# Kernel tuning notes

Hardware: AMD Instinct MI355X
Metric: run time of the kernel (lower is better)

Reference implementation:

```python
import jax, jax.numpy as jnp
import numpy as np

NROW = 200000
R = 32
B = 131072
NDIM = 3
STEP = 0.01  # stepsize from optimize() default step=lambda x: 0.01


def setup_inputs() -> dict:
    key = jax.random.key(0)
    ks = jax.random.split(key, 12)
    inp = {}
    for d in range(NDIM):
        # positive entries (like torch.rand) keep phi > 0
        inp[f"U{d}"] = jax.random.uniform(ks[d], (NROW, R), dtype=jnp.float32, minval=0.05, maxval=1.0)
        inp[f"S{d}"] = jax.random.uniform(ks[3 + d], (NROW, R), dtype=jnp.float32)
        inp[f"T{d}"] = jax.random.uniform(ks[6 + d], (NROW, R), dtype=jnp.float32)
    inp["L"] = jax.random.uniform(ks[9], (R,), dtype=jnp.float32, minval=0.1, maxval=1.0)
    inp["batch_vals"] = jax.random.randint(ks[10], (B,), 0, 2).astype(jnp.float32)  # binary data
    inp["batch_entries"] = jax.random.randint(ks[11], (B, NDIM), 0, NROW)
    return inp


def _em_update(U, S, T, L, batch_vals, batch_entries):
    # U, S, T: (ndim, nrow, R); batch_entries: (B, ndim); batch_vals: (B,)
    idx = batch_entries.T  # (ndim, B)
    g = jax.vmap(lambda u, i: u[i])(U, idx)  # gathered rows: (ndim, B, R)
    # c_vectors[dim] = L * prod of OTHER dims' gathered vectors
    prod_others = jnp.stack([g[1] * g[2], g[0] * g[2], g[0] * g[1]])  # (ndim, B, R)
    c = L * prod_others  # (ndim, B, R)
    p = g[0] * g[1] * g[2]  # (B, R) full elementwise product
    phi = jnp.sum(L * p, axis=-1)  # (B,)
    # d_vectors[dim, b, r] = phi[b] - L[r] * p[b, r]  (same for every dim)
    d_vec = (phi[:, None] - L * p)[None]  # (1, B, R)
    # expectation step (binary): E[wi] = 0.5/phi * tanh(phi/2)
    wi = 0.5 / phi * jnp.tanh(phi / 2.0)  # (B,)
    ki = batch_vals - 0.5  # (B,)
    wi_b = wi[None, :, None]
    s_upd = c * c * wi_b  # (ndim, B, R)
    t_upd = (ki[None, :, None] - d_vec * wi_b) * c  # (ndim, B, R)
    seg = lambda dat, i: jax.ops.segment_sum(dat, i, num_segments=NROW)
    s_acc = jax.vmap(seg)(s_upd, idx)  # (ndim, NROW, R)
    t_acc = jax.vmap(seg)(t_upd, idx)
    cnt = jax.vmap(seg)(jnp.ones(idx.shape, jnp.float32), idx)  # (ndim, NROW)
    touched = (cnt > 0)[..., None]
    # EMA write-back only to rows that appeared in the batch
    S_new = jnp.where(touched, (1.0 - STEP) * S + STEP * s_acc, S)
    T_new = jnp.where(touched, (1.0 - STEP) * T + STEP * t_acc, T)
    return jnp.stack([S_new, T_new])  # (2, ndim, NROW, R)


def reference(U0, U1, U2, S0, S1, S2, T0, T1, T2, L, batch_vals, batch_entries):
    U = jnp.stack([U0, U1, U2])
    S = jnp.stack([S0, S1, S2])
    T = jnp.stack([T0, T1, T2])
    return _em_update(U, S, T, L, batch_vals, batch_entries)
```

## Files before the change

### kernel.cpp

```cpp
#include <hip/hip_runtime.h>

#define NROW 200000
#define RDIM 32
#define BATCH 131072
#define STEP 0.01f
#define CAPB 4
#define ROWS3 (3 * NROW)


__device__ __forceinline__ unsigned f2bf(float x) {
    unsigned u = __float_as_uint(x);
    return (u + 0x8000u) >> 16;
}
__device__ __forceinline__ float bf2f(unsigned h) {
    return __uint_as_float(h << 16);
}

__global__ __launch_bounds__(256) void em_pre_v11(
    const float* __restrict__ U0, const float* __restrict__ U1,
    const float* __restrict__ U2, const float* __restrict__ L,
    const float* __restrict__ bv, const int* __restrict__ be,
    int* __restrict__ cnt, int* __restrict__ head, int* __restrict__ nxt,
    int* __restrict__ bucket2, float2* __restrict__ scal, float* __restrict__ LpBuf)
{
    int tid = blockIdx.x * blockDim.x + threadIdx.x;
    int i   = tid >> 3;
    int sub = tid & 7;
    if (i >= BATCH) return;

    int e0 = be[i * 3 + 0];
    int e1 = be[i * 3 + 1];
    int e2 = be[i * 3 + 2];

    float4 g0 = *(const float4*)(U0 + (size_t)e0 * RDIM + sub * 4);
    float4 g1 = *(const float4*)(U1 + (size_t)e1 * RDIM + sub * 4);
    float4 g2 = *(const float4*)(U2 + (size_t)e2 * RDIM + sub * 4);
    float4 Lv = *(const float4*)(L + sub * 4);

    float4 Lp;
    Lp.x = Lv.x * g0.x * g1.x * g2.x;
    Lp.y = Lv.y * g0.y * g1.y * g2.y;
    Lp.z = Lv.z * g0.z * g1.z * g2.z;
    Lp.w = Lv.w * g0.w * g1.w * g2.w;

    float phi = (Lp.x + Lp.y) + (Lp.z + Lp.w);
    phi += __shfl_xor(phi, 1);
    phi += __shfl_xor(phi, 2);
    phi += __shfl_xor(phi, 4);

    float wi = 0.5f / phi * tanhf(0.5f * phi);
    float A  = (bv[i] - 0.5f) - phi * wi;

    *(float4*)(LpBuf + (size_t)i * RDIM + sub * 4) = Lp;

    if (sub == 0) scal[i] = make_float2(A, wi);

    if (sub < 3) {
        int row  = (sub == 0) ? e0 : (sub == 1) ? e1 : e2;
        int rid  = sub * NROW + row;
        int slot = atomicAdd(&cnt[rid], 1);
        if (slot < CAPB) {
            int packed = (int)((f2bf(A) << 16) | f2bf(wi));
            *(int2*)(bucket2 + (size_t)rid * 8 + slot * 2) = make_int2(i, packed);
        } else {
            int idx = i * 3 + sub;
            nxt[idx] = atomicExch(&head[rid], idx + 1);
        }
    }
}

#define ACCS(SA, TA, RG, Aj, Wj, P)                                     \
{                                                                       \
    float cx = (P).x * (RG).x, cy = (P).y * (RG).y,                     \
          cz = (P).z * (RG).z, cw = (P).w * (RG).w;                     \
    (SA).x += (Wj) * cx * cx;  (SA).y += (Wj) * cy * cy;                \
    (SA).z += (Wj) * cz * cz;  (SA).w += (Wj) * cw * cw;                \
    (TA).x += ((Aj) + (Wj) * (P).x) * cx;                               \
    (TA).y += ((Aj) + (Wj) * (P).y) * cy;                               \
    (TA).z += ((Aj) + (Wj) * (P).z) * cz;                               \
    (TA).w += ((Aj) + (Wj) * (P).w) * cw;                               \
}

__global__ __launch_bounds__(256) void em_apply_v11(
    const float* __restrict__ U0, const float* __restrict__ U1,
    const float* __restrict__ U2,
    const float* __restrict__ S0, const float* __restrict__ S1,
    const float* __restrict__ S2,
    const float* __restrict__ T0, const float* __restrict__ T1,
    const float* __restrict__ T2,
    const int* __restrict__ cnt, const int* __restrict__ head,
    const int* __restrict__ nxt, const int* __restrict__ bucket2,
    const float2* __restrict__ scal, const float* __restrict__ LpBuf,
    float* __restrict__ out)
{
    int tid = blockIdx.x * blockDim.x + threadIdx.x;
    int rid = tid >> 3;
    int sub = tid & 7;
    if (rid >= ROWS3) return;

    int d   = rid / NROW;
    int row = rid - d * NROW;

    const float* Ud   = (d == 0) ? U0 : (d == 1) ? U1 : U2;
    const float* Ssrc = (d == 0) ? S0 : (d == 1) ? S1 : S2;
    const float* Tsrc = (d == 0) ? T0 : (d == 1) ? T1 : T2;

    size_t roff = (size_t)row * RDIM + sub * 4;

    int    n    = cnt[rid];
    const int* brow = bucket2 + (size_t)rid * 8;
    int4   b01  = *(const int4*)(brow);
    int4   b23  = *(const int4*)(brow + 4);
    float4 s_in = *(const float4*)(Ssrc + roff);
    float4 t_in = *(const float4*)(Tsrc + roff);

    int i0 = (n > 0) ? b01.x : 0;
    int i1 = (n > 1) ? b01.z : 0;
    int i2 = (n > 2) ? b23.x : 0;
    int i3 = (n > 3) ? b23.z : 0;

    float4 p0 = *(const float4*)(LpBuf + (size_t)i0 * RDIM + sub * 4);
    float4 p1 = *(const float4*)(LpBuf + (size_t)i1 * RDIM + sub * 4);
    float4 p2 = *(const float4*)(LpBuf + (size_t)i2 * RDIM + sub * 4);
    float4 p3 = *(const float4*)(LpBuf + (size_t)i3 * RDIM + sub * 4);

    float A0 = bf2f(((unsigned)b01.y) >> 16), W0 = bf2f(((unsigned)b01.y) & 0xffffu);
    float A1 = bf2f(((unsigned)b01.w) >> 16), W1 = bf2f(((unsigned)b01.w) & 0xffffu);
    float A2 = bf2f(((unsigned)b23.y) >> 16), W2 = bf2f(((unsigned)b23.y) & 0xffffu);
    float A3 = bf2f(((unsigned)b23.w) >> 16), W3 = bf2f(((unsigned)b23.w) & 0xffffu);
    if (n <= 1) { A1 = 0.f; W1 = 0.f; }
    if (n <= 2) { A2 = 0.f; W2 = 0.f; }
    if (n <= 3) { A3 = 0.f; W3 = 0.f; }

    float4 rg = make_float4(0.f, 0.f, 0.f, 0.f);
    if (n > 0) {
        float4 gd = *(const float4*)(Ud + roff);
        rg.x = __builtin_amdgcn_rcpf(gd.x);
        rg.y = __builtin_amdgcn_rcpf(gd.y);
        rg.z = __builtin_amdgcn_rcpf(gd.z);
        rg.w = __builtin_amdgcn_rcpf(gd.w);
    }

    float4 sa = make_float4(0.f, 0.f, 0.f, 0.f);
    float4 ta = make_float4(0.f, 0.f, 0.f, 0.f);

    ACCS(sa, ta, rg, A0, W0, p0)
    ACCS(sa, ta, rg, A1, W1, p1)
    ACCS(sa, ta, rg, A2, W2, p2)
    ACCS(sa, ta, rg, A3, W3, p3)

    if (n > CAPB) {
        int t = head[rid];
        while (t != 0) {
            int idx = t - 1;
            int e   = idx / 3;
            float2 aw = scal[e];
            float4 P  = *(const float4*)(LpBuf + (size_t)e * RDIM + sub * 4);
            ACCS(sa, ta, rg, aw.x, aw.y, P)
            t = nxt[idx];
        }
    }

    bool touched = (n > 0);
    float4 oS, oT;
    oS.x = touched ? (1.0f - STEP) * s_in.x + STEP * sa.x : s_in.x;
    oS.y = touched ? (1.0f - STEP) * s_in.y + STEP * sa.y : s_in.y;
    oS.z = touched ? (1.0f - STEP) * s_in.z + STEP * sa.z : s_in.z;
    oS.w = touched ? (1.0f - STEP) * s_in.w + STEP * sa.w : s_in.w;
    oT.x = touched ? (1.0f - STEP) * t_in.x + STEP * ta.x : t_in.x;
    oT.y = touched ? (1.0f - STEP) * t_in.y + STEP * ta.y : t_in.y;
    oT.z = touched ? (1.0f - STEP) * t_in.z + STEP * ta.z : t_in.z;
    oT.w = touched ? (1.0f - STEP) * t_in.w + STEP * ta.w : t_in.w;

    size_t off = (size_t)rid * RDIM + sub * 4;
    *(float4*)(out + off) = oS;
    *(float4*)(out + (size_t)ROWS3 * RDIM + off) = oT;
}

__global__ __launch_bounds__(256) void em_pre(
    const float* __restrict__ U0, const float* __restrict__ U1,
    const float* __restrict__ U2, const float* __restrict__ L,
    const float* __restrict__ bv, const int* __restrict__ be,
    int* __restrict__ head, int* __restrict__ nxt,
    float2* __restrict__ scal, float* __restrict__ LpBuf)
{
    int tid = blockIdx.x * blockDim.x + threadIdx.x;
    int i   = tid >> 3;
    int sub = tid & 7;
    if (i >= BATCH) return;

    int e0 = be[i * 3 + 0];
    int e1 = be[i * 3 + 1];
    int e2 = be[i * 3 + 2];

    float4 g0 = *(const float4*)(U0 + (size_t)e0 * RDIM + sub * 4);
    float4 g1 = *(const float4*)(U1 + (size_t)e1 * RDIM + sub * 4);
    float4 g2 = *(const float4*)(U2 + (size_t)e2 * RDIM + sub * 4);
    float4 Lv = *(const float4*)(L + sub * 4);

    float4 Lp;
    Lp.x = Lv.x * g0.x * g1.x * g2.x;
    Lp.y = Lv.y * g0.y * g1.y * g2.y;
    Lp.z = Lv.z * g0.z * g1.z * g2.z;
    Lp.w = Lv.w * g0.w * g1.w * g2.w;

    float phi = (Lp.x + Lp.y) + (Lp.z + Lp.w);
    phi += __shfl_xor(phi, 1);
    phi += __shfl_xor(phi, 2);
    phi += __shfl_xor(phi, 4);

    float wi = 0.5f / phi * tanhf(0.5f * phi);

    *(float4*)(LpBuf + (size_t)i * RDIM + sub * 4) = Lp;

    if (sub == 0) {
        float A = (bv[i] - 0.5f) - phi * wi;
        scal[i] = make_float2(A, wi);
    }
    if (sub < 3) {
        int row = (sub == 0) ? e0 : (sub == 1) ? e1 : e2;
        int idx = i * 3 + sub;
        nxt[idx] = atomicExch(&head[sub * NROW + row], idx + 1);
    }
}

__global__ __launch_bounds__(256) void em_apply_vec(
    const float* __restrict__ U0, const float* __restrict__ U1,
    const float* __restrict__ U2,
    const float* __restrict__ S0, const float* __restrict__ S1,
    const float* __restrict__ S2,
    const float* __restrict__ T0, const float* __restrict__ T1,
    const float* __restrict__ T2,
    const int* __restrict__ head, const int* __restrict__ nxt,
    const float2* __restrict__ scal, const float* __restrict__ LpBuf,
    float* __restrict__ out)
{
    int tid = blockIdx.x * blockDim.x + threadIdx.x;
    int rid = tid >> 3;
    int sub = tid & 7;
    if (rid >= ROWS3) return;

    int d   = rid / NROW;
    int row = rid - d * NROW;

    const float* Ud   = (d == 0) ? U0 : (d == 1) ? U1 : U2;
    const float* Ssrc = (d == 0) ? S0 : (d == 1) ? S1 : S2;
    const float* Tsrc = (d == 0) ? T0 : (d == 1) ? T1 : T2;

    size_t roff = (size_t)row * RDIM + sub * 4;
    float4 s_in = *(const float4*)(Ssrc + roff);
    float4 t_in = *(const float4*)(Tsrc + roff);

    int    t  = head[rid];
    float4 oS = s_in;
    float4 oT = t_in;

    if (t != 0) {
        float4 gd = *(const float4*)(Ud + roff);
        float4 rg;
        rg.x = __builtin_amdgcn_rcpf(gd.x);
        rg.y = __builtin_amdgcn_rcpf(gd.y);
        rg.z = __builtin_amdgcn_rcpf(gd.z);
        rg.w = __builtin_amdgcn_rcpf(gd.w);

        float4 sa = make_float4(0.f, 0.f, 0.f, 0.f);
        float4 ta = make_float4(0.f, 0.f, 0.f, 0.f);
        while (t != 0) {
            int idx = t - 1;
            int e = idx / 3;
            float2 aw = scal[e];
            float4 Lp = *(const float4*)(LpBuf + (size_t)e * RDIM + sub * 4);
            ACCS(sa, ta, rg, aw.x, aw.y, Lp)
            t = nxt[idx];
        }
        oS.x = (1.0f - STEP) * s_in.x + STEP * sa.x;
        oS.y = (1.0f - STEP) * s_in.y + STEP * sa.y;
        oS.z = (1.0f - STEP) * s_in.z + STEP * sa.z;
        oS.w = (1.0f - STEP) * s_in.w + STEP * sa.w;
        oT.x = (1.0f - STEP) * t_in.x + STEP * ta.x;
        oT.y = (1.0f - STEP) * t_in.y + STEP * ta.y;
        oT.z = (1.0f - STEP) * t_in.z + STEP * ta.z;
        oT.w = (1.0f - STEP) * t_in.w + STEP * ta.w;
    }

    size_t offS = (size_t)rid * RDIM + sub * 4;
    *(float4*)(out + offS) = oS;
    *(float4*)(out + (size_t)ROWS3 * RDIM + offS) = oT;
}

extern "C" void kernel_launch(void* const* d_in, const int* in_sizes, int n_in,
                              void* d_out, int out_size, void* d_ws, size_t ws_size,
                              hipStream_t stream)
{
    const float* U0 = (const float*)d_in[0];
    const float* S0 = (const float*)d_in[1];
    const float* T0 = (const float*)d_in[2];
    const float* U1 = (const float*)d_in[3];
    const float* S1 = (const float*)d_in[4];
    const float* T1 = (const float*)d_in[5];
    const float* U2 = (const float*)d_in[6];
    const float* S2 = (const float*)d_in[7];
    const float* T2 = (const float*)d_in[8];
    const float* L  = (const float*)d_in[9];
    const float* bv = (const float*)d_in[10];
    const int*   be = (const int*)d_in[11];

    float* out = (float*)d_out;

    const size_t rows3 = (size_t)ROWS3;
    const size_t nxt_n = (size_t)3 * BATCH;
    const size_t bk2_n = rows3 * 8;

    const size_t ws_fast = (2 * rows3 + nxt_n + bk2_n) * sizeof(int)
                         + (size_t)BATCH * sizeof(float2)
                         + (size_t)BATCH * RDIM * sizeof(float);
    const size_t ws_mid  = (rows3 + nxt_n) * sizeof(int)
                         + (size_t)BATCH * sizeof(float2)
                         + (size_t)BATCH * RDIM * sizeof(float);

    if (ws_size >= ws_fast) {
        int*    cnt     = (int*)d_ws;
        int*    head_   = cnt + rows3;
        int*    nxt     = head_ + rows3;
        int*    bucket2 = nxt + nxt_n;
        float2* scal    = (float2*)(bucket2 + bk2_n);
        float*  LpBuf   = (float*)(scal + BATCH);

        hipMemsetAsync(cnt, 0, 2 * rows3 * sizeof(int), stream);

        int pblocks = (BATCH * 8 + 255) / 256;
        em_pre_v11<<<pblocks, 256, 0, stream>>>(U0, U1, U2, L, bv, be,
                                                cnt, head_, nxt, bucket2,
                                                scal, LpBuf);

        long athreads = (long)ROWS3 * 8;
        int  ablocks  = (int)((athreads + 255) / 256);
        em_apply_v11<<<ablocks, 256, 0, stream>>>(U0, U1, U2, S0, S1, S2,
                                                  T0, T1, T2, cnt, head_, nxt,
                                                  bucket2, scal, LpBuf, out);
    } else if (ws_size >= ws_mid) {
        int*    head_ = (int*)d_ws;
        int*    nxt   = head_ + rows3;
        float2* scal  = (float2*)(nxt + nxt_n);
        float*  LpBuf = (float*)(scal + BATCH);

        hipMemsetAsync(head_, 0, rows3 * sizeof(int), stream);

        int pblocks = (BATCH * 8 + 255) / 256;
        em_pre<<<pblocks, 256, 0, stream>>>(U0, U1, U2, L, bv, be,
                                            head_, nxt, scal, LpBuf);

        long athreads = (long)ROWS3 * 8;
        int  ablocks  = (int)((athreads + 255) / 256);
        em_apply_vec<<<ablocks, 256, 0, stream>>>(U0, U1, U2, S0, S1, S2,
                                                  T0, T1, T2, head_, nxt,
                                                  scal, LpBuf, out);
    }
}
```

Baseline: 107.0 us.

## Precompute per-entry bf16 S/T contributions into fat buckets in pre kernel

The pre kernel now computes the full per-entry S and T contributions (wi*c^2 and (A+wi*Lp)*c) for the first CAPB occurrences of each row. It stores them packed as bf16 pairs in a fat per-row bucket array. The apply kernel then just sums up to four uint4 loads per lane and skips the U reload and reciprocal unless a row overflows into the linked list. This trades a much larger workspace (rows3*CAPB*128 bytes) and extra bf16 rounding of the contributions for less gather-dependent work in the apply pass. It only takes effect if the provided workspace is large enough.

```diff
diff --git a/kernel.cpp b/kernel.cpp
--- a/kernel.cpp
+++ b/kernel.cpp
@@ -12,8 +12,184 @@
     unsigned u = __float_as_uint(x);
     return (u + 0x8000u) >> 16;
 }
-__device__ __forceinline__ float bf2f(unsigned h) {
-    return __uint_as_float(h << 16);
+__device__ __forceinline__ float bf2f(unsigned h) { return __uint_as_float(h << 16); }
+__device__ __forceinline__ float bfhi(unsigned u) { return __uint_as_float(u & 0xffff0000u); }
+__device__ __forceinline__ float bflo(unsigned u) { return __uint_as_float(u << 16); }
+__device__ __forceinline__ unsigned pk2(float hi, float lo) {
+    return (f2bf(hi) << 16) | f2bf(lo);
+}
+
+#define ACCS(SA, TA, RG, Aj, Wj, P)                                     \
+{                                                                       \
+    float cx = (P).x * (RG).x, cy = (P).y * (RG).y,                     \
+          cz = (P).z * (RG).z, cw = (P).w * (RG).w;                     \
+    (SA).x += (Wj) * cx * cx;  (SA).y += (Wj) * cy * cy;                \
+    (SA).z += (Wj) * cz * cz;  (SA).w += (Wj) * cw * cw;                \
+    (TA).x += ((Aj) + (Wj) * (P).x) * cx;                               \
+    (TA).y += ((Aj) + (Wj) * (P).y) * cy;                               \
+    (TA).z += ((Aj) + (Wj) * (P).z) * cz;                               \
+    (TA).w += ((Aj) + (Wj) * (P).w) * cw;                               \
+}
+
+__global__ __launch_bounds__(256) void em_pre_v12(
+    const float* __restrict__ U0, const float* __restrict__ U1,
+    const float* __restrict__ U2, const float* __restrict__ L,
+    const float* __restrict__ bv, const int* __restrict__ be,
+    int* __restrict__ cnt, int* __restrict__ head, int* __restrict__ nxt,
+    float2* __restrict__ scal, float* __restrict__ LpBuf,
+    unsigned* __restrict__ fat)
+{
+    int tid = blockIdx.x * blockDim.x + threadIdx.x;
+    int i   = tid >> 3;
+    int sub = tid & 7;
+    if (i >= BATCH) return;
+
+    int e0 = be[i * 3 + 0];
+    int e1 = be[i * 3 + 1];
+    int e2 = be[i * 3 + 2];
+
+    float4 g0 = *(const float4*)(U0 + (size_t)e0 * RDIM + sub * 4);
+    float4 g1 = *(const float4*)(U1 + (size_t)e1 * RDIM + sub * 4);
+    float4 g2 = *(const float4*)(U2 + (size_t)e2 * RDIM + sub * 4);
+    float4 Lv = *(const float4*)(L + sub * 4);
+
+    float4 Lp;
+    Lp.x = Lv.x * g0.x * g1.x * g2.x;
+    Lp.y = Lv.y * g0.y * g1.y * g2.y;
+    Lp.z = Lv.z * g0.z * g1.z * g2.z;
+    Lp.w = Lv.w * g0.w * g1.w * g2.w;
+
+    float phi = (Lp.x + Lp.y) + (Lp.z + Lp.w);
+    phi += __shfl_xor(phi, 1);
+    phi += __shfl_xor(phi, 2);
+    phi += __shfl_xor(phi, 4);
+
+    float wi = 0.5f / phi * tanhf(0.5f * phi);
+    float A  = (bv[i] - 0.5f) - phi * wi;
+
+    *(float4*)(LpBuf + (size_t)i * RDIM + sub * 4) = Lp;
+    if (sub == 0) scal[i] = make_float2(A, wi);
+
+    int slotv = 0;
+    if (sub < 3) {
+        int row = (sub == 0) ? e0 : (sub == 1) ? e1 : e2;
+        int rid = sub * NROW + row;
+        slotv = atomicAdd(&cnt[rid], 1);
+        if (slotv >= CAPB) {
+            int idx = i * 3 + sub;
+            nxt[idx] = atomicExch(&head[rid], idx + 1);
+        }
+    }
+    int s0 = __shfl(slotv, 0, 8);
+    int s1 = __shfl(slotv, 1, 8);
+    int s2 = __shfl(slotv, 2, 8);
+
+    float4 tc;
+    tc.x = A + wi * Lp.x;  tc.y = A + wi * Lp.y;
+    tc.z = A + wi * Lp.z;  tc.w = A + wi * Lp.w;
+
+    #define EMIT(SLOT, RID, CA, CB)                                         \
+    if ((SLOT) < CAPB) {                                                    \
+        float4 c;                                                           \
+        c.x = Lv.x * (CA).x * (CB).x;  c.y = Lv.y * (CA).y * (CB).y;        \
+        c.z = Lv.z * (CA).z * (CB).z;  c.w = Lv.w * (CA).w * (CB).w;        \
+        uint4 q;                                                            \
+        q.x = pk2(wi * c.x * c.x, wi * c.y * c.y);                          \
+        q.y = pk2(wi * c.z * c.z, wi * c.w * c.w);                          \
+        q.z = pk2(tc.x * c.x, tc.y * c.y);                                  \
+        q.w = pk2(tc.z * c.z, tc.w * c.w);                                  \
+        *(uint4*)(fat + ((size_t)(RID) * CAPB + (SLOT)) * 32 + sub * 4) = q;\
+    }
+
+    EMIT(s0, 0 * NROW + e0, g1, g2)
+    EMIT(s1, 1 * NROW + e1, g0, g2)
+    EMIT(s2, 2 * NROW + e2, g0, g1)
+    #undef EMIT
+}
+
+__global__ __launch_bounds__(256) void em_apply_v12(
+    const float* __restrict__ U0, const float* __restrict__ U1,
+    const float* __restrict__ U2,
+    const float* __restrict__ S0, const float* __restrict__ S1,
+    const float* __restrict__ S2,
+    const float* __restrict__ T0, const float* __restrict__ T1,
+    const float* __restrict__ T2,
+    const int* __restrict__ cnt, const int* __restrict__ head,
+    const int* __restrict__ nxt, const unsigned* __restrict__ fat,
+    const float2* __restrict__ scal, const float* __restrict__ LpBuf,
+    float* __restrict__ out)
+{
+    int tid = blockIdx.x * blockDim.x + threadIdx.x;
+    int rid = tid >> 3;
+    int sub = tid & 7;
+    if (rid >= ROWS3) return;
+
+    int d   = rid / NROW;
+    int row = rid - d * NROW;
+
+    const float* Ssrc = (d == 0) ? S0 : (d == 1) ? S1 : S2;
+    const float* Tsrc = (d == 0) ? T0 : (d == 1) ? T1 : T2;
+
+    size_t roff = (size_t)row * RDIM + sub * 4;
+
+    int    n    = cnt[rid];
+    float4 s_in = *(const float4*)(Ssrc + roff);
+    float4 t_in = *(const float4*)(Tsrc + roff);
+
+    const unsigned* fb = fat + (size_t)rid * CAPB * 32 + sub * 4;
+    uint4 q0 = make_uint4(0, 0, 0, 0);
+    uint4 q1 = q0, q2 = q0, q3 = q0;
+    if (n > 0) q0 = *(const uint4*)(fb);
+    if (n > 1) q1 = *(const uint4*)(fb + 32);
+    if (n > 2) q2 = *(const uint4*)(fb + 64);
+    if (n > 3) q3 = *(const uint4*)(fb + 96);
+
+    float4 sa = make_float4(0.f, 0.f, 0.f, 0.f);
+    float4 ta = make_float4(0.f, 0.f, 0.f, 0.f);
+
+    #define UACC(Q)                                         \
+    {                                                       \
+        sa.x += bfhi((Q).x);  sa.y += bflo((Q).x);          \
+        sa.z += bfhi((Q).y);  sa.w += bflo((Q).y);          \
+        ta.x += bfhi((Q).z);  ta.y += bflo((Q).z);          \
+        ta.z += bfhi((Q).w);  ta.w += bflo((Q).w);          \
+    }
+    UACC(q0) UACC(q1) UACC(q2) UACC(q3)
+    #undef UACC
+
+    if (n > CAPB) {
+        const float* Ud = (d == 0) ? U0 : (d == 1) ? U1 : U2;
+        float4 gd = *(const float4*)(Ud + roff);
+        float4 rg;
+        rg.x = __builtin_amdgcn_rcpf(gd.x);
+        rg.y = __builtin_amdgcn_rcpf(gd.y);
+        rg.z = __builtin_amdgcn_rcpf(gd.z);
+        rg.w = __builtin_amdgcn_rcpf(gd.w);
+        int t = head[rid];
+        while (t != 0) {
+            int idx = t - 1;
+            int e   = idx / 3;
+            float2 aw = scal[e];
+            float4 P  = *(const float4*)(LpBuf + (size_t)e * RDIM + sub * 4);
+            ACCS(sa, ta, rg, aw.x, aw.y, P)
+            t = nxt[idx];
+        }
+    }
+
+    bool touched = (n > 0);
+    float4 oS, oT;
+    oS.x = touched ? (1.0f - STEP) * s_in.x + STEP * sa.x : s_in.x;
+    oS.y = touched ? (1.0f - STEP) * s_in.y + STEP * sa.y : s_in.y;
+    oS.z = touched ? (1.0f - STEP) * s_in.z + STEP * sa.z : s_in.z;
+    oS.w = touched ? (1.0f - STEP) * s_in.w + STEP * sa.w : s_in.w;
+    oT.x = touched ? (1.0f - STEP) * t_in.x + STEP * ta.x : t_in.x;
+    oT.y = touched ? (1.0f - STEP) * t_in.y + STEP * ta.y : t_in.y;
+    oT.z = touched ? (1.0f - STEP) * t_in.z + STEP * ta.z : t_in.z;
+    oT.w = touched ? (1.0f - STEP) * t_in.w + STEP * ta.w : t_in.w;
+
+    size_t off = (size_t)rid * RDIM + sub * 4;
+    *(float4*)(out + off) = oS;
+    *(float4*)(out + (size_t)ROWS3 * RDIM + off) = oT;
 }
 
 __global__ __launch_bounds__(256) void em_pre_v11(
@@ -67,18 +243,6 @@
             nxt[idx] = atomicExch(&head[rid], idx + 1);
         }
     }
-}
-
-#define ACCS(SA, TA, RG, Aj, Wj, P)                                     \
-{                                                                       \
-    float cx = (P).x * (RG).x, cy = (P).y * (RG).y,                     \
-          cz = (P).z * (RG).z, cw = (P).w * (RG).w;                     \
-    (SA).x += (Wj) * cx * cx;  (SA).y += (Wj) * cy * cy;                \
-    (SA).z += (Wj) * cz * cz;  (SA).w += (Wj) * cw * cw;                \
-    (TA).x += ((Aj) + (Wj) * (P).x) * cx;                               \
-    (TA).y += ((Aj) + (Wj) * (P).y) * cy;                               \
-    (TA).z += ((Aj) + (Wj) * (P).z) * cz;                               \
-    (TA).w += ((Aj) + (Wj) * (P).w) * cw;                               \
 }
 
 __global__ __launch_bounds__(256) void em_apply_v11(
@@ -177,117 +341,6 @@
     *(float4*)(out + (size_t)ROWS3 * RDIM + off) = oT;
 }
 
-__global__ __launch_bounds__(256) void em_pre(
-    const float* __restrict__ U0, const float* __restrict__ U1,
-    const float* __restrict__ U2, const float* __restrict__ L,
-    const float* __restrict__ bv, const int* __restrict__ be,
-    int* __restrict__ head, int* __restrict__ nxt,
-    float2* __restrict__ scal, float* __restrict__ LpBuf)
-{
-    int tid = blockIdx.x * blockDim.x + threadIdx.x;
-    int i   = tid >> 3;
-    int sub = tid & 7;
-    if (i >= BATCH) return;
-
-    int e0 = be[i * 3 + 0];
-    int e1 = be[i * 3 + 1];
-    int e2 = be[i * 3 + 2];
-
-    float4 g0 = *(const float4*)(U0 + (size_t)e0 * RDIM + sub * 4);
-    float4 g1 = *(const float4*)(U1 + (size_t)e1 * RDIM + sub * 4);
-    float4 g2 = *(const float4*)(U2 + (size_t)e2 * RDIM + sub * 4);
-    float4 Lv = *(const float4*)(L + sub * 4);
-
-    float4 Lp;
-    Lp.x = Lv.x * g0.x * g1.x * g2.x;
-    Lp.y = Lv.y * g0.y * g1.y * g2.y;
-    Lp.z = Lv.z * g0.z * g1.z * g2.z;
-    Lp.w = Lv.w * g0.w * g1.w * g2.w;
-
-    float phi = (Lp.x + Lp.y) + (Lp.z + Lp.w);
-    phi += __shfl_xor(phi, 1);
-    phi += __shfl_xor(phi, 2);
-    phi += __shfl_xor(phi, 4);
-
-    float wi = 0.5f / phi * tanhf(0.5f * phi);
-
-    *(float4*)(LpBuf + (size_t)i * RDIM + sub * 4) = Lp;
-
-    if (sub == 0) {
-        float A = (bv[i] - 0.5f) - phi * wi;
-        scal[i] = make_float2(A, wi);
-    }
-    if (sub < 3) {
-        int row = (sub == 0) ? e0 : (sub == 1) ? e1 : e2;
-        int idx = i * 3 + sub;
-        nxt[idx] = atomicExch(&head[sub * NROW + row], idx + 1);
-    }
-}
-
-__global__ __launch_bounds__(256) void em_apply_vec(
-    const float* __restrict__ U0, const float* __restrict__ U1,
-    const float* __restrict__ U2,
-    const float* __restrict__ S0, const float* __restrict__ S1,
-    const float* __restrict__ S2,
-    const float* __restrict__ T0, const float* __restrict__ T1,
-    const float* __restrict__ T2,
-    const int* __restrict__ head, const int* __restrict__ nxt,
-    const float2* __restrict__ scal, const float* __restrict__ LpBuf,
-    float* __restrict__ out)
-{
-    int tid = blockIdx.x * blockDim.x + threadIdx.x;
-    int rid = tid >> 3;
-    int sub = tid & 7;
-    if (rid >= ROWS3) return;
-
-    int d   = rid / NROW;
-    int row = rid - d * NROW;
-
-    const float* Ud   = (d == 0) ? U0 : (d == 1) ? U1 : U2;
-    const float* Ssrc = (d == 0) ? S0 : (d == 1) ? S1 : S2;
-    const float* Tsrc = (d == 0) ? T0 : (d == 1) ? T1 : T2;
-
-    size_t roff = (size_t)row * RDIM + sub * 4;
-    float4 s_in = *(const float4*)(Ssrc + roff);
-    float4 t_in = *(const float4*)(Tsrc + roff);
-
-    int    t  = head[rid];
-    float4 oS = s_in;
-    float4 oT = t_in;
-
-    if (t != 0) {
-        float4 gd = *(const float4*)(Ud + roff);
-        float4 rg;
-        rg.x = __builtin_amdgcn_rcpf(gd.x);
-        rg.y = __builtin_amdgcn_rcpf(gd.y);
-        rg.z = __builtin_amdgcn_rcpf(gd.z);
-        rg.w = __builtin_amdgcn_rcpf(gd.w);
-
-        float4 sa = make_float4(0.f, 0.f, 0.f, 0.f);
-        float4 ta = make_float4(0.f, 0.f, 0.f, 0.f);
-        while (t != 0) {
-            int idx = t - 1;
-            int e = idx / 3;
-            float2 aw = scal[e];
-            float4 Lp = *(const float4*)(LpBuf + (size_t)e * RDIM + sub * 4);
-            ACCS(sa, ta, rg, aw.x, aw.y, Lp)
-            t = nxt[idx];
-        }
-        oS.x = (1.0f - STEP) * s_in.x + STEP * sa.x;
-        oS.y = (1.0f - STEP) * s_in.y + STEP * sa.y;
-        oS.z = (1.0f - STEP) * s_in.z + STEP * sa.z;
-        oS.w = (1.0f - STEP) * s_in.w + STEP * sa.w;
-        oT.x = (1.0f - STEP) * t_in.x + STEP * ta.x;
-        oT.y = (1.0f - STEP) * t_in.y + STEP * ta.y;
-        oT.z = (1.0f - STEP) * t_in.z + STEP * ta.z;
-        oT.w = (1.0f - STEP) * t_in.w + STEP * ta.w;
-    }
-
-    size_t offS = (size_t)rid * RDIM + sub * 4;
-    *(float4*)(out + offS) = oS;
-    *(float4*)(out + (size_t)ROWS3 * RDIM + offS) = oT;
-}
-
 extern "C" void kernel_launch(void* const* d_in, const int* in_sizes, int n_in,
                               void* d_out, int out_size, void* d_ws, size_t ws_size,
                               hipStream_t stream)
@@ -309,16 +362,36 @@
 
     const size_t rows3 = (size_t)ROWS3;
     const size_t nxt_n = (size_t)3 * BATCH;
-    const size_t bk2_n = rows3 * 8;
-
-    const size_t ws_fast = (2 * rows3 + nxt_n + bk2_n) * sizeof(int)
-                         + (size_t)BATCH * sizeof(float2)
-                         + (size_t)BATCH * RDIM * sizeof(float);
-    const size_t ws_mid  = (rows3 + nxt_n) * sizeof(int)
-                         + (size_t)BATCH * sizeof(float2)
-                         + (size_t)BATCH * RDIM * sizeof(float);
-
-    if (ws_size >= ws_fast) {
+
+    const size_t ws_v12 = (2 * rows3 + nxt_n) * sizeof(int)
+                        + (size_t)BATCH * sizeof(float2)
+                        + (size_t)BATCH * RDIM * sizeof(float)
+                        + rows3 * CAPB * 32 * sizeof(unsigned);
+    const size_t bk2_n  = rows3 * 8;
+    const size_t ws_v11 = (2 * rows3 + nxt_n + bk2_n) * sizeof(int)
+                        + (size_t)BATCH * sizeof(float2)
+                        + (size_t)BATCH * RDIM * sizeof(float);
+
+    int pblocks = (BATCH * 8 + 255) / 256;
+    long athreads = (long)ROWS3 * 8;
+    int  ablocks  = (int)((athreads + 255) / 256);
+
+    if (ws_size >= ws_v12) {
+        int*      cnt   = (int*)d_ws;
+        int*      head_ = cnt + rows3;
+        int*      nxt   = head_ + rows3;
+        float2*   scal  = (float2*)(nxt + nxt_n);
+        float*    LpBuf = (float*)(scal + BATCH);
+        unsigned* fat   = (unsigned*)(LpBuf + (size_t)BATCH * RDIM);
+
+        hipMemsetAsync(cnt, 0, 2 * rows3 * sizeof(int), stream);
+
+        em_pre_v12<<<pblocks, 256, 0, stream>>>(U0, U1, U2, L, bv, be,
+                                                cnt, head_, nxt, scal, LpBuf, fat);
+        em_apply_v12<<<ablocks, 256, 0, stream>>>(U0, U1, U2, S0, S1, S2,
+                                                  T0, T1, T2, cnt, head_, nxt,
+                                                  fat, scal, LpBuf, out);
+    } else if (ws_size >= ws_v11) {
         int*    cnt     = (int*)d_ws;
         int*    head_   = cnt + rows3;
         int*    nxt     = head_ + rows3;
@@ -328,32 +401,11 @@
 
         hipMemsetAsync(cnt, 0, 2 * rows3 * sizeof(int), stream);
 
-        int pblocks = (BATCH * 8 + 255) / 256;
         em_pre_v11<<<pblocks, 256, 0, stream>>>(U0, U1, U2, L, bv, be,
                                                 cnt, head_, nxt, bucket2,
                                                 scal, LpBuf);
-
-        long athreads = (long)ROWS3 * 8;
-        int  ablocks  = (int)((athreads + 255) / 256);
         em_apply_v11<<<ablocks, 256, 0, stream>>>(U0, U1, U2, S0, S1, S2,
                                                   T0, T1, T2, cnt, head_, nxt,
                                                   bucket2, scal, LpBuf, out);
-    } else if (ws_size >= ws_mid) {
-        int*    head_ = (int*)d_ws;
-        int*    nxt   = head_ + rows3;
-        float2* scal  = (float2*)(nxt + nxt_n);
-        float*  LpBuf = (float*)(scal + BATCH);
-
-        hipMemsetAsync(head_, 0, rows3 * sizeof(int), stream);
-
-        int pblocks = (BATCH * 8 + 255) / 256;
-        em_pre<<<pblocks, 256, 0, stream>>>(U0, U1, U2, L, bv, be,
-                                            head_, nxt, scal, LpBuf);
-
-        long athreads = (long)ROWS3 * 8;
-        int  ablocks  = (int)((athreads + 255) / 256);
-        em_apply_vec<<<ablocks, 256, 0, stream>>>(U0, U1, U2, S0, S1, S2,
-                                                  T0, T1, T2, head_, nxt,
-                                                  scal, LpBuf, out);
-    }
-}
+    }
+}
```

Measured after the change: 106.0 us. Within noise of the previous version (-0.9%).
